# Kernel optimization log

Measured on AMD Instinct MI355X. Metric: run time of the kernel, lower is better.

## Reference

```python
import jax, jax.numpy as jnp
import numpy as np
from jax import lax

NEG = -1e9  # stand-in for -inf that keeps gradients finite
T, V, L = 2048, 32000, 8


def setup_inputs() -> dict:
    key = jax.random.key(0)
    k1, k2, k3 = jax.random.split(key, 3)
    # log piece probabilities (valid distribution in log space)
    log_piece_probs = jax.nn.log_softmax(jax.random.normal(k1, (V,), dtype=jnp.float32))
    # match_idx[t, j] = vocab index of the (unique) piece matching sequence[t:t+j+1], or -1
    match_idx = jax.random.randint(k2, (T, L), 0, V, dtype=jnp.int32)
    keep = jax.random.uniform(k3, (T, L)) < 0.3
    keep = keep.at[:, 0].set(True)  # length-1 (single char) pieces always match -> segmentable
    in_range = (jnp.arange(T)[:, None] + jnp.arange(1, L + 1)[None, :]) <= T
    match_idx = jnp.where(keep & in_range, match_idx, -1)
    return {"log_piece_probs": log_piece_probs, "match_idx": match_idx}


def _forward(log_piece_probs, match_idx):
    T_, L_ = match_idx.shape
    V_ = log_piece_probs.shape[0]
    valid = match_idx >= 0
    # w[t, j] = log p(piece matching at pos t with length j+1), NEG if no match
    w = jnp.where(valid, log_piece_probs[jnp.clip(match_idx, 0)], NEG)  # [T, L]
    # wrev[r, j] = w[r - j, j]: contribution ending at position n = r+1 from length j+1
    wrev = jnp.stack(
        [jnp.pad(w[:, j], (j, 0), constant_values=NEG)[:T_] for j in range(L_)], axis=1
    )  # [T, L]

    # forward pass: alpha[n] = logsumexp_l alpha[n-l] + w[n-l, l-1], rolling buffer of last L alphas
    def astep(buf, wr):
        a = jax.nn.logsumexp(buf[::-1] + wr)  # buf[::-1][j] = alpha[n-1-j]
        return jnp.concatenate([buf[1:], a[None]]), a

    abuf0 = jnp.concatenate([jnp.full((L_ - 1,), NEG, jnp.float32), jnp.zeros((1,), jnp.float32)])
    _, a_rest = lax.scan(astep, abuf0, wrev)
    alpha = jnp.concatenate([jnp.zeros((1,), jnp.float32), a_rest])  # [T+1], alpha[0]=0

    # backward pass: beta[t] = logsumexp_l w[t, l-1] + beta[t+l], rolling buffer of next L betas
    def bstep(buf, wt):
        b = jax.nn.logsumexp(wt + buf)  # buf[j] = beta[t+1+j]
        return jnp.concatenate([b[None], buf[:-1]]), b

    bbuf0 = jnp.concatenate([jnp.zeros((1,), jnp.float32), jnp.full((L_ - 1,), NEG, jnp.float32)])
    _, b_rest = lax.scan(bstep, bbuf0, w, reverse=True)
    beta = jnp.concatenate([b_rest, jnp.zeros((1,), jnp.float32)])  # [T+1], beta[T]=0

    # posterior: P[t, i] = exp(alpha[t] + log p_i + beta[t+len] - alpha[T])
    nxt = jnp.arange(T_)[:, None] + jnp.arange(1, L_ + 1)[None, :]  # [T, L]
    beta_next = beta[jnp.clip(nxt, 0, T_)]
    logP = alpha[:T_, None] + w + beta_next - alpha[T_]
    vals = jnp.where(valid, jnp.exp(logP), 0.0)  # [T, L]
    P = jnp.zeros((T_, V_), jnp.float32).at[
        jnp.arange(T_)[:, None], jnp.clip(match_idx, 0)
    ].add(vals)
    return P


def reference(log_piece_probs, match_idx):
    return _forward(log_piece_probs, match_idx)
```

## Files before the change

kernel.cpp:

```cpp
#include <hip/hip_runtime.h>


#define NEGV -1e9f
#define LOG2E 1.4426950408889634f
constexpr int T = 2048;
constexpr int L = 8;
constexpr int V = 32000;
constexpr int NCH = 64;
constexpr int K = 32;
constexpr int BLK = 256;
constexpr int FILLB = 4096;
constexpr int N4 = T * V / 4;
constexpr int CH4 = N4 / FILLB;

typedef float vfloat4 __attribute__((ext_vector_type(4)));

__device__ __forceinline__ float hexp2(float x) { return __builtin_amdgcn_exp2f(x); }
__device__ __forceinline__ float hlog2(float x) { return __builtin_amdgcn_logf(x); }

__device__ __forceinline__ float lse8v(float t0, float t1, float t2, float t3,
                                       float t4, float t5, float t6, float t7) {
    float m = fmaxf(fmaxf(fmaxf(t0, t1), fmaxf(t2, t3)),
                    fmaxf(fmaxf(t4, t5), fmaxf(t6, t7)));
    float s = hexp2(t0 - m) + hexp2(t1 - m) + hexp2(t2 - m) + hexp2(t3 - m)
            + hexp2(t4 - m) + hexp2(t5 - m) + hexp2(t6 - m) + hexp2(t7 - m);
    return m + hlog2(s);
}

__global__ __launch_bounds__(BLK) void scan_fill_kernel(
        const float* __restrict__ logp, const int* __restrict__ midx,
        float* __restrict__ out, float* __restrict__ alpha, float* __restrict__ beta,
        float* __restrict__ wf, float* __restrict__ wb) {
    const int tid = threadIdx.x;
    const int bx = blockIdx.x;

    if (bx >= 2) {
        vfloat4 z = (vfloat4)0.f;
        vfloat4* o4 = (vfloat4*)out;
        const int base4 = (bx - 2) * CH4;
        const int end4 = base4 + CH4;
        for (int i = base4 + tid; i < end4; i += BLK)
            __builtin_nontemporal_store(z, &o4[i]);
        return;
    }

    __shared__ __align__(16) float sPm[NCH * 64];
    __shared__ float sVst[(NCH + 1) * 8];

    float* w = (bx == 0) ? wf : wb;
    if (bx == 0) {
        for (int oo = tid; oo < T * 2; oo += BLK) {
            int r = oo >> 1, j0 = (oo & 1) * 4;
            vfloat4 v;
#pragma unroll
            for (int u = 0; u < 4; ++u) {
                int j = j0 + u, t = r - j;
                float x = NEGV;
                if (t >= 0) { int m = midx[(t << 3) + j]; if (m >= 0) x = logp[m] * LOG2E; }
                v[u] = x;
            }
            ((vfloat4*)wf)[oo] = v;
        }
        if (tid == 0) alpha[0] = 0.f;
    } else {
        for (int oo = tid; oo < T * 2; oo += BLK) {
            int s = oo >> 1, j0 = (oo & 1) * 4, t = T - 1 - s;
            vfloat4 v;
#pragma unroll
            for (int u = 0; u < 4; ++u) {
                int m = midx[(t << 3) + j0 + u];
                v[u] = (m >= 0) ? logp[m] * LOG2E : NEGV;
            }
            ((vfloat4*)wb)[oo] = v;
        }
        if (tid == 0) beta[T] = 0.f;
    }
    __syncthreads();

    {
        const int c = tid >> 2, sub = tid & 3;
        float q0[8], q1[8];
#pragma unroll
        for (int i = 0; i < 8; ++i) {
            q0[i] = (i == sub) ? 0.f : NEGV;
            q1[i] = (i == sub + 4) ? 0.f : NEGV;
        }
        const float4* wr4 = (const float4*)(w + c * K * 8);
        float4 c0 = wr4[0], c1 = wr4[1];
        float4 b0 = wr4[2], b1 = wr4[3];
        for (int k = 0; k < K; ++k) {
            float4 a0, a1;
            if (k + 2 < K) { a0 = wr4[(k + 2) * 2]; a1 = wr4[(k + 2) * 2 + 1]; }
            float top0 = lse8v(c0.x + q0[0], c0.y + q0[1], c0.z + q0[2], c0.w + q0[3],
                               c1.x + q0[4], c1.y + q0[5], c1.z + q0[6], c1.w + q0[7]);
            float top1 = lse8v(c0.x + q1[0], c0.y + q1[1], c0.z + q1[2], c0.w + q1[3],
                               c1.x + q1[4], c1.y + q1[5], c1.z + q1[6], c1.w + q1[7]);
#pragma unroll
            for (int i = 7; i > 0; --i) { q0[i] = q0[i - 1]; q1[i] = q1[i - 1]; }
            q0[0] = top0; q1[0] = top1;
            c0 = b0; c1 = b1; b0 = a0; b1 = a1;
        }
#pragma unroll
        for (int i = 0; i < 8; ++i) {
            sPm[c * 64 + i * 8 + sub] = q0[i];
            sPm[c * 64 + i * 8 + sub + 4] = q1[i];
        }
    }
    __syncthreads();

    if (tid < 8) {
        const int r = tid;
        float v = (r == 0) ? 0.f : NEGV;
        float4 r0 = *(const float4*)&sPm[r * 8];
        float4 r1 = *(const float4*)&sPm[r * 8 + 4];
        for (int cc = 0; cc < NCH; ++cc) {
            sVst[cc * 8 + r] = v;
            float4 n0, n1;
            if (cc + 1 < NCH) {
                n0 = *(const float4*)&sPm[(cc + 1) * 64 + r * 8];
                n1 = *(const float4*)&sPm[(cc + 1) * 64 + r * 8 + 4];
            }
            float vb0 = __shfl(v, 0, 8), vb1 = __shfl(v, 1, 8);
            float vb2 = __shfl(v, 2, 8), vb3 = __shfl(v, 3, 8);
            float vb4 = __shfl(v, 4, 8), vb5 = __shfl(v, 5, 8);
            float vb6 = __shfl(v, 6, 8), vb7 = __shfl(v, 7, 8);
            v = lse8v(r0.x + vb0, r0.y + vb1, r0.z + vb2, r0.w + vb3,
                      r1.x + vb4, r1.y + vb5, r1.z + vb6, r1.w + vb7);
            r0 = n0; r1 = n1;
        }
        sVst[NCH * 8 + r] = v;
    }
    __syncthreads();

    if (tid < NCH) {
        const int cc = tid;
        float ab[8];
#pragma unroll
        for (int i = 0; i < 8; ++i) ab[i] = sVst[cc * 8 + i];
        const float4* wr4 = (const float4*)(w + cc * K * 8);
        float4 c0 = wr4[0], c1 = wr4[1];
        float4 b0 = wr4[2], b1 = wr4[3];
        for (int k = 0; k < K; ++k) {
            float4 a0, a1;
            if (k + 2 < K) { a0 = wr4[(k + 2) * 2]; a1 = wr4[(k + 2) * 2 + 1]; }
            float val = lse8v(c0.x + ab[0], c0.y + ab[1], c0.z + ab[2], c0.w + ab[3],
                              c1.x + ab[4], c1.y + ab[5], c1.z + ab[6], c1.w + ab[7]);
            int s = cc * K + k;
            if (bx == 0) alpha[s + 1] = val;
            else         beta[T - 1 - s] = val;
#pragma unroll
            for (int i = 7; i > 0; --i) ab[i] = ab[i - 1];
            ab[0] = val;
            c0 = b0; c1 = b1; b0 = a0; b1 = a1;
        }
    }
}

__global__ __launch_bounds__(256) void scatter_kernel(
        const float* __restrict__ logp, const int* __restrict__ midx,
        float* __restrict__ out, const float* __restrict__ alpha,
        const float* __restrict__ beta) {
    int i = blockIdx.x * blockDim.x + threadIdx.x;
    if (i >= T * L) return;
    int m = midx[i];
    if (m < 0) return;
    int t = i >> 3, j = i & 7;
    int nx = t + j + 1;
    if (nx > T) nx = T;
    float lp2 = alpha[t] + logp[m] * LOG2E + beta[nx] - alpha[T];
    atomicAdd(&out[(size_t)t * V + m], hexp2(lp2));
}

extern "C" void kernel_launch(void* const* d_in, const int* in_sizes, int n_in,
                              void* d_out, int out_size, void* d_ws, size_t ws_size,
                              hipStream_t stream) {
    const float* logp = (const float*)d_in[0];
    const int*   midx = (const int*)d_in[1];
    float* out = (float*)d_out;

    float* ws    = (float*)d_ws;
    float* alpha = ws;
    float* beta  = alpha + 2064;
    float* wf    = beta + 2064;
    float* wb    = wf + 16384;

    scan_fill_kernel<<<dim3(2 + FILLB), BLK, 0, stream>>>(logp, midx, out, alpha, beta, wf, wb);
    scatter_kernel<<<dim3((T * L) / 256), 256, 0, stream>>>(logp, midx, out, alpha, beta);
}
```

Baseline: 323.8 us.

## Use 512-thread blocks, one column per thread in chunk scan, stage outputs in LDS

```diff
diff --git a/kernel.cpp b/kernel.cpp
--- a/kernel.cpp
+++ b/kernel.cpp
@@ -8,7 +8,7 @@
 constexpr int V = 32000;
 constexpr int NCH = 64;
 constexpr int K = 32;
-constexpr int BLK = 256;
+constexpr int BLK = 512;
 constexpr int FILLB = 4096;
 constexpr int N4 = T * V / 4;
 constexpr int CH4 = N4 / FILLB;
@@ -35,17 +35,17 @@
     const int bx = blockIdx.x;
 
     if (bx >= 2) {
-        vfloat4 z = (vfloat4)0.f;
-        vfloat4* o4 = (vfloat4*)out;
+        float4 z = make_float4(0.f, 0.f, 0.f, 0.f);
+        float4* o4 = (float4*)out;
         const int base4 = (bx - 2) * CH4;
         const int end4 = base4 + CH4;
-        for (int i = base4 + tid; i < end4; i += BLK)
-            __builtin_nontemporal_store(z, &o4[i]);
+        for (int i = base4 + tid; i < end4; i += BLK) o4[i] = z;
         return;
     }
 
     __shared__ __align__(16) float sPm[NCH * 64];
     __shared__ float sVst[(NCH + 1) * 8];
+    __shared__ float sOut[NCH * 33];
 
     float* w = (bx == 0) ? wf : wb;
     if (bx == 0) {
@@ -61,7 +61,6 @@
             }
             ((vfloat4*)wf)[oo] = v;
         }
-        if (tid == 0) alpha[0] = 0.f;
     } else {
         for (int oo = tid; oo < T * 2; oo += BLK) {
             int s = oo >> 1, j0 = (oo & 1) * 4, t = T - 1 - s;
@@ -73,38 +72,29 @@
             }
             ((vfloat4*)wb)[oo] = v;
         }
-        if (tid == 0) beta[T] = 0.f;
     }
     __syncthreads();
 
     {
-        const int c = tid >> 2, sub = tid & 3;
-        float q0[8], q1[8];
+        const int c = tid >> 3, col = tid & 7;
+        float q[8];
 #pragma unroll
-        for (int i = 0; i < 8; ++i) {
-            q0[i] = (i == sub) ? 0.f : NEGV;
-            q1[i] = (i == sub + 4) ? 0.f : NEGV;
-        }
+        for (int i = 0; i < 8; ++i) q[i] = (i == col) ? 0.f : NEGV;
         const float4* wr4 = (const float4*)(w + c * K * 8);
         float4 c0 = wr4[0], c1 = wr4[1];
         float4 b0 = wr4[2], b1 = wr4[3];
         for (int k = 0; k < K; ++k) {
             float4 a0, a1;
             if (k + 2 < K) { a0 = wr4[(k + 2) * 2]; a1 = wr4[(k + 2) * 2 + 1]; }
-            float top0 = lse8v(c0.x + q0[0], c0.y + q0[1], c0.z + q0[2], c0.w + q0[3],
-                               c1.x + q0[4], c1.y + q0[5], c1.z + q0[6], c1.w + q0[7]);
-            float top1 = lse8v(c0.x + q1[0], c0.y + q1[1], c0.z + q1[2], c0.w + q1[3],
-                               c1.x + q1[4], c1.y + q1[5], c1.z + q1[6], c1.w + q1[7]);
+            float top = lse8v(c0.x + q[0], c0.y + q[1], c0.z + q[2], c0.w + q[3],
+                              c1.x + q[4], c1.y + q[5], c1.z + q[6], c1.w + q[7]);
 #pragma unroll
-            for (int i = 7; i > 0; --i) { q0[i] = q0[i - 1]; q1[i] = q1[i - 1]; }
-            q0[0] = top0; q1[0] = top1;
+            for (int i = 7; i > 0; --i) q[i] = q[i - 1];
+            q[0] = top;
             c0 = b0; c1 = b1; b0 = a0; b1 = a1;
         }
 #pragma unroll
-        for (int i = 0; i < 8; ++i) {
-            sPm[c * 64 + i * 8 + sub] = q0[i];
-            sPm[c * 64 + i * 8 + sub + 4] = q1[i];
-        }
+        for (int i = 0; i < 8; ++i) sPm[c * 64 + i * 8 + col] = q[i];
     }
     __syncthreads();
 
@@ -145,14 +135,25 @@
             if (k + 2 < K) { a0 = wr4[(k + 2) * 2]; a1 = wr4[(k + 2) * 2 + 1]; }
             float val = lse8v(c0.x + ab[0], c0.y + ab[1], c0.z + ab[2], c0.w + ab[3],
                               c1.x + ab[4], c1.y + ab[5], c1.z + ab[6], c1.w + ab[7]);
-            int s = cc * K + k;
-            if (bx == 0) alpha[s + 1] = val;
-            else         beta[T - 1 - s] = val;
+            sOut[cc * 33 + k] = val;
 #pragma unroll
             for (int i = 7; i > 0; --i) ab[i] = ab[i - 1];
             ab[0] = val;
             c0 = b0; c1 = b1; b0 = a0; b1 = a1;
         }
+    }
+    __syncthreads();
+
+    if (bx == 0) {
+        for (int o = tid; o < T; o += BLK)
+            alpha[o + 1] = sOut[(o >> 5) * 33 + (o & 31)];
+        if (tid == 0) alpha[0] = 0.f;
+    } else {
+        for (int o = tid; o < T; o += BLK) {
+            int s = T - 1 - o;
+            beta[o] = sOut[(s >> 5) * 33 + (s & 31)];
+        }
+        if (tid == 0) beta[T] = 0.f;
     }
 }
 
```

New measurement: 294.6 us. 9.0% less time.
